# Optimization experiments

Hardware: AMD Instinct MI355X
Metric: run time of the kernel (lower is better)

The kernel has to match this reference:

```python
import jax, jax.numpy as jnp
import numpy as np

HEADS = 8
DIM_HEAD = 64
SCALE = DIM_HEAD ** (-0.5)
EPS = 1e-5


def setup_inputs() -> dict:
    key = jax.random.key(0)
    k1, k2, k3, k4 = jax.random.split(key, 4)
    b, c, t = 16, 512, 4096
    hidden = HEADS * DIM_HEAD
    x = jax.random.normal(k1, (b, c, t), dtype=jnp.float32)
    W_qkv = jax.random.normal(k2, (hidden * 3, c), dtype=jnp.float32) * (c ** -0.5)
    W_out = jax.random.normal(k3, (c, hidden), dtype=jnp.float32) * (hidden ** -0.5)
    b_out = jax.random.normal(k4, (c,), dtype=jnp.float32) * 0.02
    gn_w = jnp.ones((c,), dtype=jnp.float32)
    gn_b = jnp.zeros((c,), dtype=jnp.float32)
    return {"x": x, "W_qkv": W_qkv, "W_out": W_out, "b_out": b_out,
            "gn_w": gn_w, "gn_b": gn_b}


def reference(x, W_qkv, W_out, b_out, gn_w, gn_b):
    b, c, t = x.shape
    # 1x1 conv = channel matmul: [3*hidden, c] @ [b, c, t] -> [b, 3*hidden, t]
    qkv = jnp.einsum('oc,bct->bot', W_qkv, x)
    q, k, v = jnp.split(qkv, 3, axis=1)
    q = q.reshape(b, HEADS, DIM_HEAD, t)
    k = k.reshape(b, HEADS, DIM_HEAD, t)
    v = v.reshape(b, HEADS, DIM_HEAD, t)
    q = jax.nn.softmax(q, axis=-2) * SCALE  # softmax over feature dim
    k = jax.nn.softmax(k, axis=-1)          # softmax over time dim
    # context = k @ v^T : [b,h,dk,t] x [b,h,t,dv] -> [b,h,dk,dv]
    context = jnp.einsum('bhdt,bhet->bhde', k, v)
    # out = context^T @ q : [b,h,dv,dk] x [b,h,dk,t] -> [b,h,dv,t]
    out = jnp.einsum('bhde,bhdt->bhet', context, q)
    out = out.reshape(b, HEADS * DIM_HEAD, t)
    # output 1x1 conv with bias
    out = jnp.einsum('oc,bct->bot', W_out, out) + b_out[None, :, None]
    # GroupNorm(1, dim): normalize over (channels, time) per sample
    mean = jnp.mean(out, axis=(1, 2), keepdims=True)
    var = jnp.var(out, axis=(1, 2), keepdims=True)
    out = (out - mean) * jax.lax.rsqrt(var + EPS)
    out = out * gn_w[None, :, None] + gn_b[None, :, None]
    return out
```

## Files before the change

kernel.cpp:

```cpp
#include <hip/hip_runtime.h>
#include <stdint.h>

#define B_ 16
#define C_ 512
#define T_ 4096
#define H_ 8
#define D_ 64
#define SCALE_ 0.125f
#define EPS_ 1e-5f

using ushortT = unsigned short;
using ushort8 = __attribute__((ext_vector_type(8))) unsigned short;
using short8  = __attribute__((ext_vector_type(8))) short;
using floatx4 = __attribute__((ext_vector_type(4))) float;

__device__ __forceinline__ float bf2f(ushortT u) {
  union { unsigned int i; float f; } x; x.i = ((unsigned int)u) << 16; return x.f;
}
__device__ __forceinline__ ushortT f2bf(float f) {
  union { float f; unsigned int i; } x; x.f = f;
  unsigned int r = x.i + 0x7fffu + ((x.i >> 16) & 1u);
  return (ushortT)(r >> 16);
}

#define GLD16(gp, lp)                                                          \
  __builtin_amdgcn_global_load_lds(                                            \
      (const __attribute__((address_space(1))) unsigned int*)(gp),             \
      (__attribute__((address_space(3))) unsigned int*)(lp), 16, 0, 0)

__global__ __launch_bounds__(256) void cvt_f32_bf16(const float* __restrict__ src,
                                                    ushortT* __restrict__ dst, int n4) {
  int i = blockIdx.x * 256 + threadIdx.x;
  if (i >= n4) return;
  floatx4 v = *(const floatx4*)(src + (size_t)i * 4);
  unsigned int p0 = (unsigned int)f2bf(v[0]) | ((unsigned int)f2bf(v[1]) << 16);
  unsigned int p1 = (unsigned int)f2bf(v[2]) | ((unsigned int)f2bf(v[3]) << 16);
  *(unsigned long long*)(dst + (size_t)i * 4) =
      (unsigned long long)p0 | ((unsigned long long)p1 << 32);
}

__global__ void zero_f32(float* p, int n4) {
  int i = blockIdx.x * 256 + threadIdx.x;
  if (i < n4) ((floatx4*)p)[i] = (floatx4){0.f, 0.f, 0.f, 0.f};
}

__global__ __launch_bounds__(256) void transpose_x(const float* __restrict__ x,
                                                   ushortT* __restrict__ xT) {
  __shared__ ushortT tile[64][65];
  int b = blockIdx.z;
  int t0 = blockIdx.x * 64, c0 = blockIdx.y * 64;
  const float* xb = x + (size_t)b * C_ * T_;
  ushortT* xTb = xT + (size_t)b * T_ * C_;
  for (int i = threadIdx.x; i < 4096; i += 256) {
    int cc = i >> 6, tt = i & 63;
    tile[cc][tt] = f2bf(xb[(size_t)(c0 + cc) * T_ + t0 + tt]);
  }
  __syncthreads();
  for (int i = threadIdx.x; i < 4096; i += 256) {
    int tt = i >> 6, cc = i & 63;
    xTb[(size_t)(t0 + tt) * C_ + c0 + cc] = tile[cc][tt];
  }
}

__global__ __launch_bounds__(256) void gemm_bt(
    const ushortT* __restrict__ A, const ushortT* __restrict__ Bt,
    void* __restrict__ Cc, const float* __restrict__ bias,
    int K, int lda, int ldb, int ldc, int out_f32,
    unsigned long long bsA, unsigned long long bsB, unsigned long long bsC) {
  __shared__ ushortT As[128 * 32];
  __shared__ ushortT Bs[128 * 32];
  const int b = blockIdx.z;
  A += (size_t)b * bsA; Bt += (size_t)b * bsB;
  const int m0 = blockIdx.y * 128, n0 = blockIdx.x * 128;
  const int tid = threadIdx.x;
  const int w = tid >> 6, l = tid & 63;
  const int wm = (w >> 1) * 64, wn = (w & 1) * 64;
  const int quad = l >> 4, ln = l & 15;
  floatx4 acc[4][4];
#pragma unroll
  for (int i = 0; i < 4; i++)
#pragma unroll
    for (int j = 0; j < 4; j++) acc[i][j] = (floatx4){0.f, 0.f, 0.f, 0.f};

  for (int kb = 0; kb < K; kb += 32) {
#pragma unroll
    for (int i = 0; i < 2; ++i) {
      int wci = i * 256 + (tid & 192);
      int ci  = wci + (tid & 63);
      int row = ci >> 2, col = (ci & 3) << 3;
      GLD16(&A[(size_t)(m0 + row) * lda + kb + col], &As[wci * 8]);
      GLD16(&Bt[(size_t)(n0 + row) * ldb + kb + col], &Bs[wci * 8]);
    }
    __syncthreads();
    short8 af[4], bfv[4];
#pragma unroll
    for (int i = 0; i < 4; i++) af[i] = *(const short8*)(&As[(wm + i * 16 + ln) * 32 + quad * 8]);
#pragma unroll
    for (int j = 0; j < 4; j++) bfv[j] = *(const short8*)(&Bs[(wn + j * 16 + ln) * 32 + quad * 8]);
#pragma unroll
    for (int i = 0; i < 4; i++)
#pragma unroll
      for (int j = 0; j < 4; j++)
        acc[i][j] = __builtin_amdgcn_mfma_f32_16x16x32_bf16(af[i], bfv[j], acc[i][j], 0, 0, 0);
    __syncthreads();
  }
  if (out_f32) {
    float* Co = (float*)Cc + (size_t)b * bsC;
#pragma unroll
    for (int i = 0; i < 4; i++)
#pragma unroll
      for (int r = 0; r < 4; r++) {
        int row = m0 + wm + i * 16 + quad * 4 + r;
        float bv = bias ? bias[row] : 0.f;
#pragma unroll
        for (int j = 0; j < 4; j++) {
          int col = n0 + wn + j * 16 + ln;
          Co[(size_t)row * ldc + col] = acc[i][j][r] + bv;
        }
      }
  } else {
    ushortT* Co = (ushortT*)Cc + (size_t)b * bsC;
#pragma unroll
    for (int i = 0; i < 4; i++)
#pragma unroll
      for (int r = 0; r < 4; r++) {
        int row = m0 + wm + i * 16 + quad * 4 + r;
        float bv = bias ? bias[row] : 0.f;
#pragma unroll
        for (int j = 0; j < 4; j++) {
          int col = n0 + wn + j * 16 + ln;
          Co[(size_t)row * ldc + col] = f2bf(acc[i][j][r] + bv);
        }
      }
  }
}

__global__ __launch_bounds__(256) void softmax_q(ushortT* q) {
  int row = blockIdx.x * 4 + (threadIdx.x >> 6);
  int l = threadIdx.x & 63;
  ushortT* p = q + (size_t)row * 512 + l * 8;
  ushort8 v = *(const ushort8*)p;
  float f[8];
  float mx = -1e30f;
#pragma unroll
  for (int j = 0; j < 8; j++) { f[j] = bf2f(v[j]); mx = fmaxf(mx, f[j]); }
#pragma unroll
  for (int off = 1; off < 8; off <<= 1) mx = fmaxf(mx, __shfl_xor(mx, off));
  float s = 0.f;
#pragma unroll
  for (int j = 0; j < 8; j++) { f[j] = expf(f[j] - mx); s += f[j]; }
#pragma unroll
  for (int off = 1; off < 8; off <<= 1) s += __shfl_xor(s, off);
  float inv = SCALE_ / s;
  ushort8 o;
#pragma unroll
  for (int j = 0; j < 8; j++) o[j] = f2bf(f[j] * inv);
  *(ushort8*)p = o;
}

__global__ __launch_bounds__(256) void softmax_k(ushortT* kv) {
  int b = blockIdx.x >> 9, o = blockIdx.x & 511;
  ushortT* p = kv + ((size_t)b * 1024 + o) * T_;
  int tid = threadIdx.x, w = tid >> 6, l = tid & 63;
  float f[16];
  float mx = -1e30f;
#pragma unroll
  for (int c = 0; c < 2; ++c) {
    ushort8 v = *(const ushort8*)(p + (size_t)(c * 256 + tid) * 8);
#pragma unroll
    for (int j = 0; j < 8; j++) { f[c * 8 + j] = bf2f(v[j]); mx = fmaxf(mx, f[c * 8 + j]); }
  }
#pragma unroll
  for (int off = 1; off < 64; off <<= 1) mx = fmaxf(mx, __shfl_xor(mx, off));
  __shared__ float red[4], red2[4];
  if (l == 0) red[w] = mx;
  __syncthreads();
  mx = fmaxf(fmaxf(red[0], red[1]), fmaxf(red[2], red[3]));
  float s = 0.f;
#pragma unroll
  for (int i = 0; i < 16; i++) { f[i] = expf(f[i] - mx); s += f[i]; }
#pragma unroll
  for (int off = 1; off < 64; off <<= 1) s += __shfl_xor(s, off);
  if (l == 0) red2[w] = s;
  __syncthreads();
  s = red2[0] + red2[1] + red2[2] + red2[3];
  float inv = 1.f / s;
#pragma unroll
  for (int c = 0; c < 2; ++c) {
    ushort8 o;
#pragma unroll
    for (int j = 0; j < 8; j++) o[j] = f2bf(f[c * 8 + j] * inv);
    *(ushort8*)(p + (size_t)(c * 256 + tid) * 8) = o;
  }
}

__global__ __launch_bounds__(64) void context_kv(const ushortT* __restrict__ kv,
                                                 float* __restrict__ ct) {
  __shared__ ushortT Vs[64 * 32];
  __shared__ ushortT Ks[64 * 32];
  const int slice = blockIdx.x, h = blockIdx.y, b = blockIdx.z;
  const int t0 = slice * 512;
  const ushortT* vrow = kv + ((size_t)b * 1024 + 512 + h * 64) * T_;
  const ushortT* krow = kv + ((size_t)b * 1024 + h * 64) * T_;
  const int tid = threadIdx.x, quad = tid >> 4, ln = tid & 15;
  floatx4 acc[4][4];
#pragma unroll
  for (int i = 0; i < 4; i++)
#pragma unroll
    for (int j = 0; j < 4; j++) acc[i][j] = (floatx4){0.f, 0.f, 0.f, 0.f};
  for (int kb = 0; kb < 512; kb += 32) {
#pragma unroll
    for (int i = 0; i < 4; ++i) {
      int ci = i * 64 + tid;
      int row = ci >> 2, col = (ci & 3) << 3;
      *(uint4*)(&Vs[row * 32 + col]) = *(const uint4*)(&vrow[(size_t)row * T_ + t0 + kb + col]);
      *(uint4*)(&Ks[row * 32 + col]) = *(const uint4*)(&krow[(size_t)row * T_ + t0 + kb + col]);
    }
    __syncthreads();
    short8 af[4], bfv[4];
#pragma unroll
    for (int i = 0; i < 4; i++) af[i] = *(const short8*)(&Vs[(i * 16 + ln) * 32 + quad * 8]);
#pragma unroll
    for (int j = 0; j < 4; j++) bfv[j] = *(const short8*)(&Ks[(j * 16 + ln) * 32 + quad * 8]);
#pragma unroll
    for (int i = 0; i < 4; i++)
#pragma unroll
      for (int j = 0; j < 4; j++)
        acc[i][j] = __builtin_amdgcn_mfma_f32_16x16x32_bf16(af[i], bfv[j], acc[i][j], 0, 0, 0);
    __syncthreads();
  }
  float* ctbh = ct + (size_t)(b * 8 + h) * 4096;
#pragma unroll
  for (int i = 0; i < 4; i++)
#pragma unroll
    for (int r = 0; r < 4; r++) {
      int e = i * 16 + quad * 4 + r;
#pragma unroll
      for (int j = 0; j < 4; j++) {
        int d = j * 16 + ln;
        atomicAdd(&ctbh[e * 64 + d], acc[i][j][r]);
      }
    }
}

__global__ __launch_bounds__(64) void attn_out(const ushortT* __restrict__ qT,
                                               const float* __restrict__ ct,
                                               ushortT* __restrict__ attT) {
  __shared__ ushortT Qs[64 * 64];
  __shared__ ushortT Cs[64 * 64];
  const int t0 = blockIdx.x * 64, h = blockIdx.y, b = blockIdx.z;
  const int tid = threadIdx.x, quad = tid >> 4, ln = tid & 15;
  const ushortT* qb = qT + (size_t)b * T_ * 512;
  const float* ctbh = ct + (size_t)(b * 8 + h) * 4096;
#pragma unroll
  for (int i = 0; i < 8; ++i) {
    int ci = i * 64 + tid;
    int row = ci >> 3, col = (ci & 7) << 3;
    *(uint4*)(&Qs[row * 64 + col]) = *(const uint4*)(&qb[(size_t)(t0 + row) * 512 + h * 64 + col]);
  }
#pragma unroll
  for (int i = 0; i < 16; ++i) {
    int ci = i * 64 + tid;
    int off = ci * 4, row = off >> 6, col = off & 63;
    floatx4 v = *(const floatx4*)(&ctbh[off]);
    unsigned int p0 = (unsigned int)f2bf(v[0]) | ((unsigned int)f2bf(v[1]) << 16);
    unsigned int p1 = (unsigned int)f2bf(v[2]) | ((unsigned int)f2bf(v[3]) << 16);
    *(unsigned long long*)(&Cs[row * 64 + col]) =
        (unsigned long long)p0 | ((unsigned long long)p1 << 32);
  }
  __syncthreads();
  floatx4 acc[4][4];
#pragma unroll
  for (int i = 0; i < 4; i++)
#pragma unroll
    for (int j = 0; j < 4; j++) acc[i][j] = (floatx4){0.f, 0.f, 0.f, 0.f};
#pragma unroll
  for (int kk = 0; kk < 2; ++kk) {
    short8 af[4], bfv[4];
#pragma unroll
    for (int i = 0; i < 4; i++) af[i] = *(const short8*)(&Qs[(i * 16 + ln) * 64 + kk * 32 + quad * 8]);
#pragma unroll
    for (int j = 0; j < 4; j++) bfv[j] = *(const short8*)(&Cs[(j * 16 + ln) * 64 + kk * 32 + quad * 8]);
#pragma unroll
    for (int i = 0; i < 4; i++)
#pragma unroll
      for (int j = 0; j < 4; j++)
        acc[i][j] = __builtin_amdgcn_mfma_f32_16x16x32_bf16(af[i], bfv[j], acc[i][j], 0, 0, 0);
  }
  ushortT* ob = attT + (size_t)b * T_ * 512;
#pragma unroll
  for (int i = 0; i < 4; i++)
#pragma unroll
    for (int r = 0; r < 4; r++) {
      int row = t0 + i * 16 + quad * 4 + r;
#pragma unroll
      for (int j = 0; j < 4; j++) {
        int col = h * 64 + j * 16 + ln;
        ob[(size_t)row * 512 + col] = f2bf(acc[i][j][r]);
      }
    }
}

__global__ __launch_bounds__(256) void gn_stats(const float* __restrict__ out,
                                                float* __restrict__ stats) {
  int b = blockIdx.y;
  const float* p = out + (size_t)b * C_ * T_;
  float s = 0.f, ss = 0.f;
  for (int i = blockIdx.x * 256 + threadIdx.x; i < C_ * T_ / 8; i += 32 * 256) {
    floatx4 v0 = *(const floatx4*)(p + (size_t)i * 8);
    floatx4 v1 = *(const floatx4*)(p + (size_t)i * 8 + 4);
#pragma unroll
    for (int j = 0; j < 4; j++) { s += v0[j]; ss += v0[j] * v0[j]; }
#pragma unroll
    for (int j = 0; j < 4; j++) { s += v1[j]; ss += v1[j] * v1[j]; }
  }
#pragma unroll
  for (int off = 1; off < 64; off <<= 1) { s += __shfl_xor(s, off); ss += __shfl_xor(ss, off); }
  __shared__ float rs[4], rss[4];
  int w = threadIdx.x >> 6, l = threadIdx.x & 63;
  if (l == 0) { rs[w] = s; rss[w] = ss; }
  __syncthreads();
  if (threadIdx.x == 0) {
    s = rs[0] + rs[1] + rs[2] + rs[3];
    ss = rss[0] + rss[1] + rss[2] + rss[3];
    atomicAdd(&stats[b * 2], s);
    atomicAdd(&stats[b * 2 + 1], ss);
  }
}

__global__ __launch_bounds__(256) void gn_apply(float* __restrict__ out,
                                                const float* __restrict__ stats,
                                                const float* __restrict__ gnw,
                                                const float* __restrict__ gnb) {
  int b = blockIdx.y;
  int i = blockIdx.x * 256 + threadIdx.x;
  const float invN = 1.f / (float)(C_ * T_);
  float mean = stats[b * 2] * invN;
  float var = stats[b * 2 + 1] * invN - mean * mean;
  float inv = rsqrtf(var + EPS_);
  int c = i >> 9;
  float wv = gnw[c] * inv, bv = gnb[c];
  float* p = out + (size_t)b * C_ * T_ + (size_t)i * 8;
  floatx4 v0 = *(const floatx4*)p;
  floatx4 v1 = *(const floatx4*)(p + 4);
#pragma unroll
  for (int j = 0; j < 4; j++) v0[j] = (v0[j] - mean) * wv + bv;
#pragma unroll
  for (int j = 0; j < 4; j++) v1[j] = (v1[j] - mean) * wv + bv;
  *(floatx4*)p = v0;
  *(floatx4*)(p + 4) = v1;
}

extern "C" void kernel_launch(void* const* d_in, const int* in_sizes, int n_in,
                              void* d_out, int out_size, void* d_ws, size_t ws_size,
                              hipStream_t stream) {
  (void)in_sizes; (void)n_in; (void)out_size; (void)ws_size;
  const float* x    = (const float*)d_in[0];
  const float* Wqkv = (const float*)d_in[1];
  const float* Wout = (const float*)d_in[2];
  const float* bout = (const float*)d_in[3];
  const float* gnw  = (const float*)d_in[4];
  const float* gnb  = (const float*)d_in[5];
  float* out = (float*)d_out;

  char* ws = (char*)d_ws;
  ushortT* xT   = (ushortT*)(ws);
  ushortT* qT   = (ushortT*)(ws + 67108864);
  ushortT* Wqbf = (ushortT*)(ws + 134217728);
  ushortT* Wobf = (ushortT*)(ws + 135790592);
  float*   ct   = (float*)(ws + 136314880);
  float* stats  = (float*)(ws + 138412032);
  ushortT* kv   = (ushortT*)d_out;
  ushortT* attT = qT;

  cvt_f32_bf16<<<768, 256, 0, stream>>>(Wqkv, Wqbf, 196608);
  cvt_f32_bf16<<<256, 256, 0, stream>>>(Wout, Wobf, 65536);
  zero_f32<<<513, 256, 0, stream>>>(ct, 131080);

  transpose_x<<<dim3(64, 8, 16), 256, 0, stream>>>(x, xT);

  gemm_bt<<<dim3(32, 8, 16), 256, 0, stream>>>(
      Wqbf + 512 * 512, xT, kv, nullptr, 512, 512, 512, 4096, 0,
      0ULL, (unsigned long long)(T_ * 512), (unsigned long long)(1024 * T_));

  gemm_bt<<<dim3(4, 32, 16), 256, 0, stream>>>(
      xT, Wqbf, qT, nullptr, 512, 512, 512, 512, 0,
      (unsigned long long)(T_ * 512), 0ULL, (unsigned long long)(T_ * 512));

  softmax_q<<<16384, 256, 0, stream>>>(qT);
  softmax_k<<<8192, 256, 0, stream>>>(kv);

  context_kv<<<dim3(8, 8, 16), 64, 0, stream>>>(kv, ct);
  attn_out<<<dim3(64, 8, 16), 64, 0, stream>>>(qT, ct, attT);

  gemm_bt<<<dim3(32, 4, 16), 256, 0, stream>>>(
      Wobf, attT, out, bout, 512, 512, 512, 4096, 1,
      0ULL, (unsigned long long)(T_ * 512), (unsigned long long)(512 * T_));

  gn_stats<<<dim3(32, 16), 256, 0, stream>>>(out, stats);
  gn_apply<<<dim3(1024, 16), 256, 0, stream>>>(out, stats, gnw, gnb);
}
```

Baseline: 642.8 us.

## Fold context into output weights, fuse q-softmax and GroupNorm stats into GEMMs

The per-batch context matrix is folded into W_out through a small fold_ct kernel, making a per-batch folded weight Wf = W_out·ctx^T. The output GEMM then consumes softmaxed q directly, which removes the attn_out kernel and its full-size intermediate. The q softmax is fused into the q projection GEMM epilogue, reducing over 64-wide head groups with shuffles. GroupNorm sum and sum-of-squares are accumulated with atomics in the output GEMM epilogue, which removes the separate gn_stats pass over the output. In exchange the output GEMM uses a per-batch weight, and the bf16 rounding order changes because the context is folded before quantization.

```diff
diff --git a/kernel.cpp b/kernel.cpp
--- a/kernel.cpp
+++ b/kernel.cpp
@@ -64,8 +64,8 @@
 
 __global__ __launch_bounds__(256) void gemm_bt(
     const ushortT* __restrict__ A, const ushortT* __restrict__ Bt,
-    void* __restrict__ Cc, const float* __restrict__ bias,
-    int K, int lda, int ldb, int ldc, int out_f32,
+    void* __restrict__ Cc, const float* __restrict__ bias, float* __restrict__ stats,
+    int K, int lda, int ldb, int ldc, int mode,
     unsigned long long bsA, unsigned long long bsB, unsigned long long bsC) {
   __shared__ ushortT As[128 * 32];
   __shared__ ushortT Bs[128 * 32];
@@ -73,8 +73,9 @@
   A += (size_t)b * bsA; Bt += (size_t)b * bsB;
   const int m0 = blockIdx.y * 128, n0 = blockIdx.x * 128;
   const int tid = threadIdx.x;
-  const int w = tid >> 6, l = tid & 63;
+  const int w = tid >> 6;
   const int wm = (w >> 1) * 64, wn = (w & 1) * 64;
+  const int l = tid & 63;
   const int quad = l >> 4, ln = l & 15;
   floatx4 acc[4][4];
 #pragma unroll
@@ -104,58 +105,62 @@
         acc[i][j] = __builtin_amdgcn_mfma_f32_16x16x32_bf16(af[i], bfv[j], acc[i][j], 0, 0, 0);
     __syncthreads();
   }
-  if (out_f32) {
-    float* Co = (float*)Cc + (size_t)b * bsC;
+
+  if (mode == 0) {
+    ushortT* Co = (ushortT*)Cc + (size_t)b * bsC;
 #pragma unroll
     for (int i = 0; i < 4; i++)
 #pragma unroll
       for (int r = 0; r < 4; r++) {
         int row = m0 + wm + i * 16 + quad * 4 + r;
-        float bv = bias ? bias[row] : 0.f;
+#pragma unroll
+        for (int j = 0; j < 4; j++)
+          Co[(size_t)row * ldc + n0 + wn + j * 16 + ln] = f2bf(acc[i][j][r]);
+      }
+  } else if (mode == 1) {
+    ushortT* Co = (ushortT*)Cc + (size_t)b * bsC;
+#pragma unroll
+    for (int i = 0; i < 4; i++)
+#pragma unroll
+      for (int r = 0; r < 4; r++) {
+        int row = m0 + wm + i * 16 + quad * 4 + r;
+        float v0 = acc[i][0][r], v1 = acc[i][1][r], v2 = acc[i][2][r], v3 = acc[i][3][r];
+        float mx = fmaxf(fmaxf(v0, v1), fmaxf(v2, v3));
+#pragma unroll
+        for (int off = 1; off < 16; off <<= 1) mx = fmaxf(mx, __shfl_xor(mx, off));
+        float e0 = expf(v0 - mx), e1 = expf(v1 - mx), e2 = expf(v2 - mx), e3 = expf(v3 - mx);
+        float s = e0 + e1 + e2 + e3;
+#pragma unroll
+        for (int off = 1; off < 16; off <<= 1) s += __shfl_xor(s, off);
+        float inv = SCALE_ / s;
+        Co[(size_t)row * ldc + n0 + wn + 0 * 16 + ln] = f2bf(e0 * inv);
+        Co[(size_t)row * ldc + n0 + wn + 1 * 16 + ln] = f2bf(e1 * inv);
+        Co[(size_t)row * ldc + n0 + wn + 2 * 16 + ln] = f2bf(e2 * inv);
+        Co[(size_t)row * ldc + n0 + wn + 3 * 16 + ln] = f2bf(e3 * inv);
+      }
+  } else {
+    float* Co = (float*)Cc + (size_t)b * bsC;
+    float s = 0.f, ss = 0.f;
+#pragma unroll
+    for (int i = 0; i < 4; i++)
+#pragma unroll
+      for (int r = 0; r < 4; r++) {
+        int row = m0 + wm + i * 16 + quad * 4 + r;
+        float bv = bias[row];
 #pragma unroll
         for (int j = 0; j < 4; j++) {
-          int col = n0 + wn + j * 16 + ln;
-          Co[(size_t)row * ldc + col] = acc[i][j][r] + bv;
+          float val = acc[i][j][r] + bv;
+          Co[(size_t)row * ldc + n0 + wn + j * 16 + ln] = val;
+          s += val; ss += val * val;
         }
       }
-  } else {
-    ushortT* Co = (ushortT*)Cc + (size_t)b * bsC;
-#pragma unroll
-    for (int i = 0; i < 4; i++)
-#pragma unroll
-      for (int r = 0; r < 4; r++) {
-        int row = m0 + wm + i * 16 + quad * 4 + r;
-        float bv = bias ? bias[row] : 0.f;
-#pragma unroll
-        for (int j = 0; j < 4; j++) {
-          int col = n0 + wn + j * 16 + ln;
-          Co[(size_t)row * ldc + col] = f2bf(acc[i][j][r] + bv);
-        }
-      }
-  }
-}
-
-__global__ __launch_bounds__(256) void softmax_q(ushortT* q) {
-  int row = blockIdx.x * 4 + (threadIdx.x >> 6);
-  int l = threadIdx.x & 63;
-  ushortT* p = q + (size_t)row * 512 + l * 8;
-  ushort8 v = *(const ushort8*)p;
-  float f[8];
-  float mx = -1e30f;
-#pragma unroll
-  for (int j = 0; j < 8; j++) { f[j] = bf2f(v[j]); mx = fmaxf(mx, f[j]); }
-#pragma unroll
-  for (int off = 1; off < 8; off <<= 1) mx = fmaxf(mx, __shfl_xor(mx, off));
-  float s = 0.f;
-#pragma unroll
-  for (int j = 0; j < 8; j++) { f[j] = expf(f[j] - mx); s += f[j]; }
-#pragma unroll
-  for (int off = 1; off < 8; off <<= 1) s += __shfl_xor(s, off);
-  float inv = SCALE_ / s;
-  ushort8 o;
-#pragma unroll
-  for (int j = 0; j < 8; j++) o[j] = f2bf(f[j] * inv);
-  *(ushort8*)p = o;
+#pragma unroll
+    for (int off = 1; off < 64; off <<= 1) { s += __shfl_xor(s, off); ss += __shfl_xor(ss, off); }
+    if (l == 0) {
+      atomicAdd(&stats[b * 2], s);
+      atomicAdd(&stats[b * 2 + 1], ss);
+    }
+  }
 }
 
 __global__ __launch_bounds__(256) void softmax_k(ushortT* kv) {
@@ -195,7 +200,7 @@
 }
 
 __global__ __launch_bounds__(64) void context_kv(const ushortT* __restrict__ kv,
-                                                 float* __restrict__ ct) {
+                                                 float* __restrict__ ct2) {
   __shared__ ushortT Vs[64 * 32];
   __shared__ ushortT Ks[64 * 32];
   const int slice = blockIdx.x, h = blockIdx.y, b = blockIdx.z;
@@ -219,9 +224,9 @@
     __syncthreads();
     short8 af[4], bfv[4];
 #pragma unroll
-    for (int i = 0; i < 4; i++) af[i] = *(const short8*)(&Vs[(i * 16 + ln) * 32 + quad * 8]);
-#pragma unroll
-    for (int j = 0; j < 4; j++) bfv[j] = *(const short8*)(&Ks[(j * 16 + ln) * 32 + quad * 8]);
+    for (int i = 0; i < 4; i++) af[i] = *(const short8*)(&Ks[(i * 16 + ln) * 32 + quad * 8]);
+#pragma unroll
+    for (int j = 0; j < 4; j++) bfv[j] = *(const short8*)(&Vs[(j * 16 + ln) * 32 + quad * 8]);
 #pragma unroll
     for (int i = 0; i < 4; i++)
 #pragma unroll
@@ -229,44 +234,34 @@
         acc[i][j] = __builtin_amdgcn_mfma_f32_16x16x32_bf16(af[i], bfv[j], acc[i][j], 0, 0, 0);
     __syncthreads();
   }
-  float* ctbh = ct + (size_t)(b * 8 + h) * 4096;
+  float* ctbh = ct2 + (size_t)(b * 8 + h) * 4096;
 #pragma unroll
   for (int i = 0; i < 4; i++)
 #pragma unroll
     for (int r = 0; r < 4; r++) {
-      int e = i * 16 + quad * 4 + r;
+      int d = i * 16 + quad * 4 + r;
 #pragma unroll
       for (int j = 0; j < 4; j++) {
-        int d = j * 16 + ln;
-        atomicAdd(&ctbh[e * 64 + d], acc[i][j][r]);
+        int e = j * 16 + ln;
+        atomicAdd(&ctbh[d * 64 + e], acc[i][j][r]);
       }
     }
 }
 
-__global__ __launch_bounds__(64) void attn_out(const ushortT* __restrict__ qT,
-                                               const float* __restrict__ ct,
-                                               ushortT* __restrict__ attT) {
-  __shared__ ushortT Qs[64 * 64];
+__global__ __launch_bounds__(64) void fold_ct(const ushortT* __restrict__ Wo,
+                                              const float* __restrict__ ct2,
+                                              ushortT* __restrict__ Wf) {
   __shared__ ushortT Cs[64 * 64];
-  const int t0 = blockIdx.x * 64, h = blockIdx.y, b = blockIdx.z;
+  const int m0 = blockIdx.x * 64, h = blockIdx.y, b = blockIdx.z;
   const int tid = threadIdx.x, quad = tid >> 4, ln = tid & 15;
-  const ushortT* qb = qT + (size_t)b * T_ * 512;
-  const float* ctbh = ct + (size_t)(b * 8 + h) * 4096;
-#pragma unroll
-  for (int i = 0; i < 8; ++i) {
-    int ci = i * 64 + tid;
-    int row = ci >> 3, col = (ci & 7) << 3;
-    *(uint4*)(&Qs[row * 64 + col]) = *(const uint4*)(&qb[(size_t)(t0 + row) * 512 + h * 64 + col]);
-  }
+  const float* cb = ct2 + (size_t)(b * 8 + h) * 4096;
 #pragma unroll
   for (int i = 0; i < 16; ++i) {
-    int ci = i * 64 + tid;
-    int off = ci * 4, row = off >> 6, col = off & 63;
-    floatx4 v = *(const floatx4*)(&ctbh[off]);
+    int off = (i * 64 + tid) * 4;
+    floatx4 v = *(const floatx4*)(cb + off);
     unsigned int p0 = (unsigned int)f2bf(v[0]) | ((unsigned int)f2bf(v[1]) << 16);
     unsigned int p1 = (unsigned int)f2bf(v[2]) | ((unsigned int)f2bf(v[3]) << 16);
-    *(unsigned long long*)(&Cs[row * 64 + col]) =
-        (unsigned long long)p0 | ((unsigned long long)p1 << 32);
+    *(unsigned long long*)(&Cs[off]) = (unsigned long long)p0 | ((unsigned long long)p1 << 32);
   }
   __syncthreads();
   floatx4 acc[4][4];
@@ -278,54 +273,27 @@
   for (int kk = 0; kk < 2; ++kk) {
     short8 af[4], bfv[4];
 #pragma unroll
-    for (int i = 0; i < 4; i++) af[i] = *(const short8*)(&Qs[(i * 16 + ln) * 64 + kk * 32 + quad * 8]);
-#pragma unroll
-    for (int j = 0; j < 4; j++) bfv[j] = *(const short8*)(&Cs[(j * 16 + ln) * 64 + kk * 32 + quad * 8]);
+    for (int i = 0; i < 4; i++)
+      af[i] = *(const short8*)(&Wo[(size_t)(m0 + i * 16 + ln) * 512 + h * 64 + kk * 32 + quad * 8]);
+#pragma unroll
+    for (int j = 0; j < 4; j++)
+      bfv[j] = *(const short8*)(&Cs[(j * 16 + ln) * 64 + kk * 32 + quad * 8]);
 #pragma unroll
     for (int i = 0; i < 4; i++)
 #pragma unroll
       for (int j = 0; j < 4; j++)
         acc[i][j] = __builtin_amdgcn_mfma_f32_16x16x32_bf16(af[i], bfv[j], acc[i][j], 0, 0, 0);
   }
-  ushortT* ob = attT + (size_t)b * T_ * 512;
+  ushortT* wfb = Wf + (size_t)b * 262144;
 #pragma unroll
   for (int i = 0; i < 4; i++)
 #pragma unroll
     for (int r = 0; r < 4; r++) {
-      int row = t0 + i * 16 + quad * 4 + r;
-#pragma unroll
-      for (int j = 0; j < 4; j++) {
-        int col = h * 64 + j * 16 + ln;
-        ob[(size_t)row * 512 + col] = f2bf(acc[i][j][r]);
-      }
-    }
-}
-
-__global__ __launch_bounds__(256) void gn_stats(const float* __restrict__ out,
-                                                float* __restrict__ stats) {
-  int b = blockIdx.y;
-  const float* p = out + (size_t)b * C_ * T_;
-  float s = 0.f, ss = 0.f;
-  for (int i = blockIdx.x * 256 + threadIdx.x; i < C_ * T_ / 8; i += 32 * 256) {
-    floatx4 v0 = *(const floatx4*)(p + (size_t)i * 8);
-    floatx4 v1 = *(const floatx4*)(p + (size_t)i * 8 + 4);
-#pragma unroll
-    for (int j = 0; j < 4; j++) { s += v0[j]; ss += v0[j] * v0[j]; }
-#pragma unroll
-    for (int j = 0; j < 4; j++) { s += v1[j]; ss += v1[j] * v1[j]; }
-  }
-#pragma unroll
-  for (int off = 1; off < 64; off <<= 1) { s += __shfl_xor(s, off); ss += __shfl_xor(ss, off); }
-  __shared__ float rs[4], rss[4];
-  int w = threadIdx.x >> 6, l = threadIdx.x & 63;
-  if (l == 0) { rs[w] = s; rss[w] = ss; }
-  __syncthreads();
-  if (threadIdx.x == 0) {
-    s = rs[0] + rs[1] + rs[2] + rs[3];
-    ss = rss[0] + rss[1] + rss[2] + rss[3];
-    atomicAdd(&stats[b * 2], s);
-    atomicAdd(&stats[b * 2 + 1], ss);
-  }
+      int c = m0 + i * 16 + quad * 4 + r;
+#pragma unroll
+      for (int j = 0; j < 4; j++)
+        wfb[(size_t)c * 512 + h * 64 + j * 16 + ln] = f2bf(acc[i][j][r]);
+    }
 }
 
 __global__ __launch_bounds__(256) void gn_apply(float* __restrict__ out,
@@ -365,38 +333,37 @@
 
   char* ws = (char*)d_ws;
   ushortT* xT   = (ushortT*)(ws);
+  ushortT* Wf   = (ushortT*)(ws);
   ushortT* qT   = (ushortT*)(ws + 67108864);
   ushortT* Wqbf = (ushortT*)(ws + 134217728);
   ushortT* Wobf = (ushortT*)(ws + 135790592);
-  float*   ct   = (float*)(ws + 136314880);
+  float*   ct2  = (float*)(ws + 136314880);
   float* stats  = (float*)(ws + 138412032);
   ushortT* kv   = (ushortT*)d_out;
-  ushortT* attT = qT;
 
   cvt_f32_bf16<<<768, 256, 0, stream>>>(Wqkv, Wqbf, 196608);
   cvt_f32_bf16<<<256, 256, 0, stream>>>(Wout, Wobf, 65536);
-  zero_f32<<<513, 256, 0, stream>>>(ct, 131080);
+  zero_f32<<<513, 256, 0, stream>>>(ct2, 131080);
 
   transpose_x<<<dim3(64, 8, 16), 256, 0, stream>>>(x, xT);
 
   gemm_bt<<<dim3(32, 8, 16), 256, 0, stream>>>(
-      Wqbf + 512 * 512, xT, kv, nullptr, 512, 512, 512, 4096, 0,
+      Wqbf + 512 * 512, xT, kv, nullptr, nullptr, 512, 512, 512, 4096, 0,
       0ULL, (unsigned long long)(T_ * 512), (unsigned long long)(1024 * T_));
 
   gemm_bt<<<dim3(4, 32, 16), 256, 0, stream>>>(
-      xT, Wqbf, qT, nullptr, 512, 512, 512, 512, 0,
+      xT, Wqbf, qT, nullptr, nullptr, 512, 512, 512, 512, 1,
       (unsigned long long)(T_ * 512), 0ULL, (unsigned long long)(T_ * 512));
 
-  softmax_q<<<16384, 256, 0, stream>>>(qT);
   softmax_k<<<8192, 256, 0, stream>>>(kv);
 
-  context_kv<<<dim3(8, 8, 16), 64, 0, stream>>>(kv, ct);
-  attn_out<<<dim3(64, 8, 16), 64, 0, stream>>>(qT, ct, attT);
+  context_kv<<<dim3(8, 8, 16), 64, 0, stream>>>(kv, ct2);
+
+  fold_ct<<<dim3(8, 8, 16), 64, 0, stream>>>(Wobf, ct2, Wf);
 
   gemm_bt<<<dim3(32, 4, 16), 256, 0, stream>>>(
-      Wobf, attT, out, bout, 512, 512, 512, 4096, 1,
-      0ULL, (unsigned long long)(T_ * 512), (unsigned long long)(512 * T_));
-
-  gn_stats<<<dim3(32, 16), 256, 0, stream>>>(out, stats);
+      Wf, qT, out, bout, stats, 512, 512, 512, 4096, 2,
+      262144ULL, (unsigned long long)(T_ * 512), (unsigned long long)(512 * T_));
+
   gn_apply<<<dim3(1024, 16), 256, 0, stream>>>(out, stats, gnw, gnb);
 }
```

Result: slower. 727.4 us (+13.2%).
